# Optimization experiments

Measured on AMD Instinct MI355X. Metric: run time of the kernel, lower is better.

Reference implementation:

```python
import jax, jax.numpy as jnp
import numpy as np

PAD, UNK, START, END = 0, 1, 2, 3


def _lstm_scan(x_tbd, Wih, Whh, b, reverse=False):
    # x_tbd: [T,B,Din]; returns all hidden states [T,B,H] and final hidden [B,H]
    B = x_tbd.shape[1]
    Hh = Whh.shape[1]
    def step(carry, xt):
        h, c = carry
        g = xt @ Wih.T + h @ Whh.T + b  # torch gate order i,f,g,o
        i, f, gg, o = jnp.split(g, 4, axis=-1)
        c = jax.nn.sigmoid(f) * c + jax.nn.sigmoid(i) * jnp.tanh(gg)
        h = jax.nn.sigmoid(o) * jnp.tanh(c)
        return (h, c), h
    z = jnp.zeros((B, Hh), x_tbd.dtype)
    (hT, _), hs = jax.lax.scan(step, (z, z), x_tbd, reverse=reverse)
    return hs, hT


def _forward(fl, input_ids, target_ids, target_lengths):
    (emb,
     eWih0f, eWhh0f, eb0f, eWih0b, eWhh0b, eb0b,
     eWih1f, eWhh1f, eb1f, eWih1b, eWhh1b, eb1b,
     dWih0, dWhh0, db0, dWih1, dWhh1, db1,
     Wenc, Wdec, Wvoc, sW, sb, ob) = fl
    V = emb.shape[0]
    B, S = input_ids.shape
    T = target_ids.shape[1]
    D = 2 * eWhh0f.shape[1]  # decoder hidden = 2*hidden_dim
    safe = lambda ids: jnp.where(ids >= V, UNK, ids)

    # ---- bidirectional 2-layer encoder ----
    x = emb[safe(input_ids)].transpose(1, 0, 2)  # [S,B,E]
    h0f, hf0T = _lstm_scan(x, eWih0f, eWhh0f, eb0f)
    h0b, hb0T = _lstm_scan(x, eWih0b, eWhh0b, eb0b, reverse=True)
    x1 = jnp.concatenate([h0f, h0b], -1)
    h1f, hf1T = _lstm_scan(x1, eWih1f, eWhh1f, eb1f)
    h1b, hb1T = _lstm_scan(x1, eWih1b, eWhh1b, eb1b, reverse=True)
    enc_hs = jnp.concatenate([h1f, h1b], -1).transpose(1, 0, 2)  # [B,S,D]
    # decoder init hidden: concat fwd/bwd final hidden per layer -> [2,B,D]
    dec_h0 = jnp.stack([jnp.concatenate([hf0T, hb0T], -1),
                        jnp.concatenate([hf1T, hb1T], -1)])

    out_proj = jnp.tanh(emb[END:] @ Wvoc)  # [V-3, 3D]
    pad_mask = input_ids == PAD
    t_range = jnp.arange(T)

    def cell(xx, h, c, Wih, Whh, b):
        g = xx @ Wih.T + h @ Whh.T + b
        i, f, gg, o = jnp.split(g, 4, -1)
        c = jax.nn.sigmoid(f) * c + jax.nn.sigmoid(i) * jnp.tanh(gg)
        return jax.nn.sigmoid(o) * jnp.tanh(c), c

    def step(carry, xs):
        h, c, cum, hist, cur, nll = carry
        t, nt = xs  # t scalar step index, nt [B] teacher tokens
        xx = emb[cur]
        h0, c0 = cell(xx, h[0], c[0], dWih0, dWhh0, db0)
        h1, c1 = cell(h0, h[1], c[1], dWih1, dWhh1, db1)
        # intra-temporal encoder attention
        s = jnp.minimum(jnp.einsum('bd,bsd->bs', h1 @ Wenc, enc_hs), 30.0)
        e = jnp.exp(s)
        temporal = e / jnp.where(t == 0, 1.0, cum + 1e-8)
        attn = jax.nn.softmax(jnp.where(pad_mask, -jnp.inf, temporal), axis=1)
        enc_ctx = jnp.einsum('bs,bsd->bd', attn, enc_hs)
        # intra-decoder attention over previous decoder hidden states
        ds = jnp.where(t_range[None, :] < t,
                       jnp.einsum('bd,ubd->bu', h1 @ Wdec, hist), -1e9)
        dec_ctx = jnp.where(t > 0,
                            jnp.einsum('bu,ubd->bd', jax.nn.softmax(ds, axis=1), hist),
                            0.0)
        concat = jnp.concatenate([h1, enc_ctx, dec_ctx], -1)  # [B,3D]
        vocab_dist = jax.nn.softmax(concat @ out_proj.T + ob, axis=1)  # [B,V-3]
        p_gen = jax.nn.sigmoid(concat @ sW.T + sb)[:, 0]
        # generation prob of teacher token (F.pad left by END zeros)
        idx = jnp.clip(nt - END, 0, V - END - 1)
        gen_p = jnp.where((nt >= END) & (nt < V),
                          jnp.take_along_axis(vocab_dist, idx[:, None], 1)[:, 0], 0.0)
        copy_p = jnp.sum(attn * (input_ids == nt[:, None]), axis=1)
        p = p_gen * gen_p + (1.0 - p_gen) * copy_p
        nll = nll - jnp.where(t < target_lengths, jnp.log(p + 1e-9), 0.0)
        return (jnp.stack([h0, h1]), jnp.stack([c0, c1]), cum + e,
                hist.at[t].set(h1), safe(nt), nll), None

    init = (dec_h0, jnp.zeros_like(dec_h0), jnp.zeros((B, S), emb.dtype),
            jnp.zeros((T, B, D), emb.dtype),
            jnp.full((B,), START), jnp.zeros((B,), emb.dtype))
    (_, _, _, _, _, nll), _ = jax.lax.scan(step, init, (t_range, target_ids.T))
    return nll  # per-example teacher-forcing NLL, shape [B]


def setup_inputs():
    key = jax.random.key(0)
    ks = jax.random.split(key, 40)
    B, S, T = 16, 512, 128
    V, E, H = 32000, 128, 256
    D = 2 * H
    inp = {}
    inp['input_ids'] = jax.random.randint(ks[0], (B, S), 4, V)      # no pad/special ids
    inp['target_ids'] = jax.random.randint(ks[1], (B, T), 4, V)
    inp['input_lengths'] = jnp.full((B,), S, dtype=jnp.int32)       # full-length (packing is identity)
    inp['target_lengths'] = jax.random.randint(ks[2], (B,), T // 2, T + 1)
    inp['max_num_oovs'] = 0
    def xav(k, shape):
        fan = shape[0] + shape[-1]
        return jax.random.normal(k, shape, jnp.float32) * np.sqrt(2.0 / fan)
    def lstm_b(n4):
        b = np.zeros(n4, np.float32)
        b[n4 // 4:n4 // 2] = 1.0  # forget-gate bias init
        return jnp.asarray(b)
    i = 3
    inp['emb'] = jax.random.uniform(ks[i], (V, E), jnp.float32, -0.1, 0.1); i += 1
    for l, din in [(0, E), (1, D)]:
        for d in 'fb':
            inp[f'enc_Wih_l{l}{d}'] = xav(ks[i], (4 * H, din)); i += 1
            inp[f'enc_Whh_l{l}{d}'] = xav(ks[i], (4 * H, H)); i += 1
            inp[f'enc_b_l{l}{d}'] = lstm_b(4 * H)
    for l, din in [(0, E), (1, D)]:
        inp[f'dec_Wih_l{l}'] = xav(ks[i], (4 * D, din)); i += 1
        inp[f'dec_Whh_l{l}'] = xav(ks[i], (4 * D, D)); i += 1
        inp[f'dec_b_l{l}'] = lstm_b(4 * D)
    inp['Wenc_attn'] = xav(ks[i], (D, D)); i += 1
    inp['Wdec_attn'] = xav(ks[i], (D, D)); i += 1
    inp['vocab_proj'] = xav(ks[i], (E, 6 * H)); i += 1
    inp['switch_W'] = xav(ks[i], (1, 6 * H)); i += 1
    inp['switch_b'] = jnp.zeros((1,), jnp.float32)
    inp['out_bias'] = jnp.zeros((V - 3,), jnp.float32)
    return inp


def reference(input_ids, target_ids, input_lengths, target_lengths, max_num_oovs,
              emb,
              enc_Wih_l0f, enc_Whh_l0f, enc_b_l0f, enc_Wih_l0b, enc_Whh_l0b, enc_b_l0b,
              enc_Wih_l1f, enc_Whh_l1f, enc_b_l1f, enc_Wih_l1b, enc_Whh_l1b, enc_b_l1b,
              dec_Wih_l0, dec_Whh_l0, dec_b_l0, dec_Wih_l1, dec_Whh_l1, dec_b_l1,
              Wenc_attn, Wdec_attn, vocab_proj, switch_W, switch_b, out_bias):
    # input_lengths unused (all full length -> pack/pad identity); max_num_oovs only
    # widens the zero-padded tail of the generator distribution (gathered probs unchanged).
    fl = (emb,
          enc_Wih_l0f, enc_Whh_l0f, enc_b_l0f, enc_Wih_l0b, enc_Whh_l0b, enc_b_l0b,
          enc_Wih_l1f, enc_Whh_l1f, enc_b_l1f, enc_Wih_l1b, enc_Whh_l1b, enc_b_l1b,
          dec_Wih_l0, dec_Whh_l0, dec_b_l0, dec_Wih_l1, dec_Whh_l1, dec_b_l1,
          Wenc_attn, Wdec_attn, vocab_proj, switch_W, switch_b, out_bias)
    return _forward(fl, input_ids, target_ids, target_lengths)
```

## Files before the change

kernel.cpp:

```cpp
#include <hip/hip_runtime.h>
#include <hip/hip_bf16.h>
#include <math.h>

#define PAD_ID 0
#define UNK_ID 1
#define START_ID 2
#define END_ID 3

constexpr int B = 16, S = 512, T = 128, V = 32000, E = 128, H = 256, D = 512;
constexpr int C3 = 1536;
constexpr int VO = 31997;
constexpr int JS = 32000;

typedef short short8 __attribute__((ext_vector_type(8)));
typedef float f32x4 __attribute__((ext_vector_type(4)));

__device__ __forceinline__ float sigm(float x) { return 1.0f / (1.0f + __expf(-x)); }
__device__ __forceinline__ short bf16s(float x) {
    __hip_bfloat16 h = __float2bfloat16(x);
    return *reinterpret_cast<short*>(&h);
}

__device__ __forceinline__ uint4 cloadu4(const uint* p) {
    uint4 v;
// ... 165 lines not shown
    int tid = threadIdx.x;
    int lane = tid & 63, w = tid >> 6;
    int cl = lane & 15, hi = lane >> 4;

    short8 afr[2][16];
    {
        int rowbase = (bk * 4 + w) * 32;
#pragma unroll
        for (int mt = 0; mt < 2; mt++)
#pragma unroll
            for (int kt = 0; kt < 16; kt++)
                afr[mt][kt] = *(const short8*)(PM + (size_t)(rowbase + mt * 16 + cl) * 512 + kt * 32 + hi * 8);
    }
    if (tid < 128) {
        int g = (tid >> 3) & 3;
        int u = (bk * 4 + (tid >> 5)) * 8 + (tid & 7);
        bias_s[tid] = bs[g * H + u];
    }
    int nl = tid >> 4, kseg = tid & 15;
    int en = tid & 15, rgrp = tid >> 4;
    for (int tt = 0; tt < 32; tt++) {
        int nt = ns * 32 + tt;
        __syncthreads();
        {
            int n = nt * 16 + nl;
            const float* src = (kseg < 8) ? (h0f + (size_t)n * H + kseg * 32)
                                          : (h0b + (size_t)n * H + (kseg - 8) * 32);
            float4 v0 = *(const float4*)(src), v1 = *(const float4*)(src + 4);
            float4 v2 = *(const float4*)(src + 8), v3 = *(const float4*)(src + 12);
            float4 v4 = *(const float4*)(src + 16), v5 = *(const float4*)(src + 20);
            float4 v6 = *(const float4*)(src + 24), v7 = *(const float4*)(src + 28);
            ushort* dst = X + nl * 520 + kseg * 32;
            st_bf8(dst, v0, v1); st_bf8(dst + 8, v2, v3);
            st_bf8(dst + 16, v4, v5); st_bf8(dst + 24, v6, v7);
        }
        __syncthreads();
        {
            f32x4 acc0 = {0.f, 0.f, 0.f, 0.f}, acc1 = {0.f, 0.f, 0.f, 0.f};
            const ushort* hp = X + cl * 520 + hi * 8;
#pragma unroll
            for (int kt = 0; kt < 16; kt++) {
                short8 bfr = *(const short8*)(hp + kt * 32);
                acc0 = __builtin_amdgcn_mfma_f32_16x16x32_bf16(afr[0][kt], bfr, acc0, 0, 0, 0);
                acc1 = __builtin_amdgcn_mfma_f32_16x16x32_bf16(afr[1][kt], bfr, acc1, 0, 0, 0);
            }
#pragma unroll
            for (int i = 0; i < 4; i++) {
                gs[w][hi * 4 + i][cl] = acc0[i];
                gs[w][16 + hi * 4 + i][cl] = acc1[i];
            }
        }
        __syncthreads();
        {
            int wv = rgrp >> 2, g = rgrp & 3;
            int u0 = (bk * 4 + wv) * 8;
            float* dst = G + (size_t)(nt * 16 + en) * 1024 + g * 256 + u0;
            float4 o0, o1;
            o0.x = gs[wv][g * 8 + 0][en] + bias_s[rgrp * 8 + 0];
            o0.y = gs[wv][g * 8 + 1][en] + bias_s[rgrp * 8 + 1];
            o0.z = gs[wv][g * 8 + 2][en] + bias_s[rgrp * 8 + 2];
            o0.w = gs[wv][g * 8 + 3][en] + bias_s[rgrp * 8 + 3];
            o1.x = gs[wv][g * 8 + 4][en] + bias_s[rgrp * 8 + 4];
            o1.y = gs[wv][g * 8 + 5][en] + bias_s[rgrp * 8 + 5];
            o1.z = gs[wv][g * 8 + 6][en] + bias_s[rgrp * 8 + 6];
            o1.w = gs[wv][g * 8 + 7][en] + bias_s[rgrp * 8 + 7];
            *(float4*)dst = o0;
            *(float4*)(dst + 4) = o1;
        }
    }
}


__device__ __forceinline__ void enc_scan_body(int blk, char* smem,
        const float* __restrict__ Gf, const float* __restrict__ Gb,
        const ushort* __restrict__ PMf, const ushort* __restrict__ PMb,
        float* __restrict__ hof, float* __restrict__ hob,
        float* __restrict__ hfin, uint* __restrict__ pk) {
    ushort* hh = (ushort*)smem;
    float (*gs)[32][17] = (float(*)[32][17])(smem + 8448);
    int dirb = blk >> 3, bk = blk & 7;
    const float* G = dirb ? Gb : Gf;
    const ushort* PM = dirb ? PMb : PMf;
    float* ho = dirb ? hob : hof;
    int tid = threadIdx.x;
    int lane = tid & 63, w = tid >> 6;
    int cl = lane & 15, hi = lane >> 4;

    short8 afr[2][8];
    {
        int rowbase = (bk * 4 + w) * 32;
#pragma unroll
        for (int mt = 0; mt < 2; mt++)
#pragma unroll
            for (int kt = 0; kt < 8; kt++)
                afr[mt][kt] = *(const short8*)(PM + (size_t)(rowbase + mt * 16 + cl) * 256 + kt * 32 + hi * 8);
    }
    int ub = tid & 31, bb = tid >> 5;
    int u_glob = bk * 32 + ub;
    int gsw = ub >> 3, ul = ub & 7;
    float c_a = 0.f, c_b = 0.f;
    int b0s = tid >> 4, u0s = (tid & 15) * 16;

    for (int step = 0; step < S; step++) {
        int s = dirb ? (S - 1 - step) : step;
        int cur = step & 1;
        const float* gA = G + ((size_t)(s * B + bb)) * 1024 + u_glob;
        const float* gB = G + ((size_t)(s * B + bb + 8)) * 1024 + u_glob;
        float pa0 = gA[0], pa1 = gA[256], pa2 = gA[512], pa3 = gA[768];
        float pb0 = gB[0], pb1 = gB[256], pb2 = gB[512], pb3 = gB[768];
        poll_stage16(pk + cur * 8192 + dirb * 4096 + tid * 16,
                     (uint)step & 0xffffu, hh + b0s * 264 + u0s);
        __syncthreads();
        {
            f32x4 acc0 = {0.f, 0.f, 0.f, 0.f}, acc1 = {0.f, 0.f, 0.f, 0.f};
            const ushort* hp = hh + cl * 264 + hi * 8;
#pragma unroll
            for (int kt = 0; kt < 8; kt++) {
                short8 bfr = *(const short8*)(hp + kt * 32);
                acc0 = __builtin_amdgcn_mfma_f32_16x16x32_bf16(afr[0][kt], bfr, acc0, 0, 0, 0);
                acc1 = __builtin_amdgcn_mfma_f32_16x16x32_bf16(afr[1][kt], bfr, acc1, 0, 0, 0);
            }
#pragma unroll
            for (int i = 0; i < 4; i++) {
                gs[w][hi * 4 + i][cl] = acc0[i];
                gs[w][16 + hi * 4 + i][cl] = acc1[i];
            }
        }
        __syncthreads();
        {
            float q0 = gs[gsw][0 + ul][bb];
            float q1 = gs[gsw][8 + ul][bb];
            float q2 = gs[gsw][16 + ul][bb];
            float q3 = gs[gsw][24 + ul][bb];
            float ig = sigm(pa0 + q0), fg = sigm(pa1 + q1), gt = tanhf(pa2 + q2), og = sigm(pa3 + q3);
            c_a = fg * c_a + ig * gt;
            float hA = og * tanhf(c_a);
            q0 = gs[gsw][0 + ul][bb + 8];
            q1 = gs[gsw][8 + ul][bb + 8];
            q2 = gs[gsw][16 + ul][bb + 8];
            q3 = gs[gsw][24 + ul][bb + 8];
            ig = sigm(pb0 + q0); fg = sigm(pb1 + q1); gt = tanhf(pb2 + q2); og = sigm(pb3 + q3);
            c_b = fg * c_b + ig * gt;
            float hB = og * tanhf(c_b);
            uint tg = (uint)(step + 1) & 0xffffu;
            uint* dstp = pk + (cur ^ 1) * 8192 + dirb * 4096;
            pstore(&dstp[bb * 256 + u_glob], ((uint)(ushort)bf16s(hA) << 16) | tg);
            pstore(&dstp[(bb + 8) * 256 + u_glob], ((uint)(ushort)bf16s(hB) << 16) | tg);
            ho[((size_t)(s * B + bb)) * H + u_glob] = hA;
            ho[((size_t)(s * B + bb + 8)) * H + u_glob] = hB;
            if (step == S - 1) {
                hfin[bb * (2 * H) + dirb * H + u_glob] = hA;
                hfin[(bb + 8) * (2 * H) + dirb * H + u_glob] = hB;
            }
        }
    }
}

__device__ __forceinline__ void dec0_body(int bid, char* smem,
        const int* __restrict__ tgt, const float* __restrict__ emb,
        const float4* __restrict__ P, const float* __restrict__ bias,
        float* __restrict__ G) {
    float (*xr)[E] = (float(*)[E])smem;
    int n0 = bid * 8;
    int tid = threadIdx.x;
    for (int i = tid; i < 8 * E; i += 256) {
        int r = i >> 7, e = i & 127;
        int n = n0 + r, t = n / B, b = n - t * B;
        int tok;
        if (t == 0) tok = START_ID;
        else { tok = tgt[b * T + (t - 1)]; if (tok >= V) tok = UNK_ID; }
        xr[r][e] = emb[(size_t)tok * E + e];
    }
    __syncthreads();
#pragma unroll
    for (int half = 0; half < 2; half++) {
        int u = tid + half * 256;
        float acc[8][4];
#pragma unroll
        for (int r = 0; r < 8; r++)
#pragma unroll
            for (int g = 0; g < 4; g++) acc[r][g] = 0.f;
#pragma unroll 4
        for (int k = 0; k < E; k++) {
            float4 w = P[k * D + u];
#pragma unroll
            for (int r = 0; r < 8; r++) {
                float x = xr[r][k];
                acc[r][0] += x * w.x; acc[r][1] += x * w.y;
                acc[r][2] += x * w.z; acc[r][3] += x * w.w;
            }
        }
        float b0 = bias[u], b1 = bias[D + u], b2 = bias[2 * D + u], b3 = bias[3 * D + u];
#pragma unroll
        for (int r = 0; r < 8; r++) {
            float* g = G + (size_t)(n0 + r) * (4 * D);
            g[u] = acc[r][0] + b0; g[D + u] = acc[r][1] + b1;
            g[2 * D + u] = acc[r][2] + b2; g[3 * D + u] = acc[r][3] + b3;
        }
    }
}

__device__ __forceinline__ void dec_body(int bk, char* smem,
        const float* __restrict__ G0, const ushort* __restrict__ PM0,
        const ushort* __restrict__ PM1, const float* __restrict__ b1,
        uint* __restrict__ h0pk, uint* __restrict__ h1pk,
        float* __restrict__ h1out) {
    ushort* hb = (ushort*)smem;
    float (*gs)[16][17] = (float(*)[16][17])(smem + 33024);
    int tid = threadIdx.x;
    int lane = tid & 63, w = tid >> 6;
    int cl = lane & 15, hi = lane >> 4;

    short8 a0[16], a1[32];
    {
        const ushort* base0 = PM0 + (size_t)(bk * 64 + w * 16 + cl) * 512 + hi * 8;
#pragma unroll
        for (int kt = 0; kt < 16; kt++) a0[kt] = *(const short8*)(base0 + kt * 32);
        const ushort* base1 = PM1 + (size_t)(bk * 64 + w * 16 + cl) * 1024 + hi * 8;
#pragma unroll
        for (int kt = 0; kt < 32; kt++) a1[kt] = *(const short8*)(base1 + kt * 32);
    }
    int u_loc = tid & 15, b = tid >> 4;
    int u = bk * 16 + u_loc;
    float bi0 = b1[u], bi1 = b1[512 + u], bi2 = b1[1024 + u], bi3 = b1[1536 + u];
    float c0v = 0.f, c1v = 0.f;
    int sb = tid >> 4, kseg = tid & 15;
    int sflat = sb * 512 + kseg * 32;

    for (int t = 0; t < T; t++) {
        int cur = t & 1;
        poll_stage32(h0pk + ((t + 1) & 1) * 8192 + sflat, (uint)(t + 1) & 0xffffu,
                     hb + sb * 1032 + kseg * 32);
        __syncthreads();
        {
            f32x4 acc = {0.f, 0.f, 0.f, 0.f};
            const ushort* hp = hb + cl * 1032 + hi * 8;
#pragma unroll
            for (int kt = 0; kt < 16; kt++) {
                short8 bfr = *(const short8*)(hp + kt * 32);
                acc = __builtin_amdgcn_mfma_f32_16x16x32_bf16(a0[kt], bfr, acc, 0, 0, 0);
            }
#pragma unroll
            for (int i = 0; i < 4; i++) gs[w][hi * 4 + i][cl] = acc[i];
        }
        __syncthreads();
        {
            const float* gg = G0 + ((size_t)(t * B + b)) * 2048 + u;
            float g0 = gg[0]    + gs[0][u_loc][b];
            float g1 = gg[512]  + gs[1][u_loc][b];
            float g2 = gg[1024] + gs[2][u_loc][b];
            float g3 = gg[1536] + gs[3][u_loc][b];
            float ig = sigm(g0), fg = sigm(g1), gt = tanhf(g2), og = sigm(g3);
            c0v = fg * c0v + ig * gt;
            float h0n = og * tanhf(c0v);
            pstore(&h0pk[cur * 8192 + b * 512 + u],
                   ((uint)(ushort)bf16s(h0n) << 16) | ((uint)(t + 2) & 0xffffu));
        }
        poll_stage32(h0pk + cur * 8192 + sflat, (uint)(t + 2) & 0xffffu,
                     hb + sb * 1032 + kseg * 32);
        poll_stage32(h1pk + ((t + 1) & 1) * 8192 + sflat, (uint)(t + 1) & 0xffffu,
                     hb + sb * 1032 + 512 + kseg * 32);
        __syncthreads();
        {
            f32x4 acc = {0.f, 0.f, 0.f, 0.f};
            const ushort* hp = hb + cl * 1032 + hi * 8;
#pragma unroll
            for (int kt = 0; kt < 32; kt++) {
                short8 bfr = *(const short8*)(hp + kt * 32);
                acc = __builtin_amdgcn_mfma_f32_16x16x32_bf16(a1[kt], bfr, acc, 0, 0, 0);
            }
#pragma unroll
            for (int i = 0; i < 4; i++) gs[w][hi * 4 + i][cl] = acc[i];
        }
        __syncthreads();
        {
            float g0 = bi0 + gs[0][u_loc][b];
            float g1 = bi1 + gs[1][u_loc][b];
            float g2 = bi2 + gs[2][u_loc][b];
            float g3 = bi3 + gs[3][u_loc][b];
            float ig = sigm(g0), fg = sigm(g1), gt = tanhf(g2), og = sigm(g3);
            c1v = fg * c1v + ig * gt;
            float h1n = og * tanhf(c1v);
            pstore(&h1pk[cur * 8192 + b * 512 + u],
                   ((uint)(ushort)bf16s(h1n) << 16) | ((uint)(t + 2) & 0xffffu));
            h1out[((size_t)(t * B + b)) * 512 + u] = h1n;
        }
        __syncthreads();
    }
}

__device__ __forceinline__ void encht2_body(int bid,
        const float* __restrict__ h1f, const float* __restrict__ h1b,
        ushort* __restrict__ enchB) {
    int idx = bid * 256 + threadIdx.x;
    int b = idx >> 15;
    int r = idx & 32767;
    int o = r >> 9, s = r & 511;
    const float* src = (o < 32) ? (h1f + ((size_t)(s * B + b)) * H + o * 8)
                                : (h1b + ((size_t)(s * B + b)) * H + (o - 32) * 8);
    float4 v0 = *(const float4*)src, v1 = *(const float4*)(src + 4);
    st_bf8(enchB + ((size_t)b << 18) + o * 4096 + s * 8, v0, v1);
}

__device__ __forceinline__ void outproj_body(int bid, char* smem,
        const float* __restrict__ emb, const float* __restrict__ Wvoc,
        __hip_bfloat16* __restrict__ outT2) {
    float (*er)[E + 1] = (float(*)[E + 1])smem;
    int j0 = bid * 32;
    int jl = threadIdx.x & 31, oq = threadIdx.x >> 5;
    for (int i = threadIdx.x; i < 32 * E; i += 256) {
        int jj = i >> 7, e = i & 127;
        int j = j0 + jj;
        er[jj][e] = (j < VO) ? emb[(size_t)(3 + j) * E + e] : 0.f;
    }
    __syncthreads();
    int j = j0 + jl;
#pragma unroll 1
    for (int i = 0; i < 24; i++) {
        int o = oq * 24 + i;
        int k0 = o * 8;
        float acc[8];
#pragma unroll
        for (int kk = 0; kk < 8; kk++) acc[kk] = 0.f;
#pragma unroll 4
        for (int e = 0; e < E; e++) {
            float x = er[jl][e];
            float4 w0 = *(const float4*)(Wvoc + (size_t)e * C3 + k0);
            float4 w1 = *(const float4*)(Wvoc + (size_t)e * C3 + k0 + 4);
            acc[0] += x * w0.x; acc[1] += x * w0.y; acc[2] += x * w0.z; acc[3] += x * w0.w;
            acc[4] += x * w1.x; acc[5] += x * w1.y; acc[6] += x * w1.z; acc[7] += x * w1.w;
        }
        short8 v;
#pragma unroll
        for (int kk = 0; kk < 8; kk++) v[kk] = bf16s(tanhf(acc[kk]));
        *reinterpret_cast<short8*>((char*)outT2 + ((size_t)o * JS + j) * 16) = v;
    }
}


__global__ void __launch_bounds__(256) megaA(
        const float* Gf, const float* Gb, const ushort* PMf, const ushort* PMb,
        float* hof, float* hob, float* hfin, uint* pk,
        const int* tgt, const float* emb, const float4* PdW, const float* dbias,
        float* Gd0) {
    __shared__ __align__(16) char smem[17152];
    int blk = blockIdx.x;
    if (blk < 16) enc_scan_body(blk, smem, Gf, Gb, PMf, PMb, hof, hob, hfin, pk);
    else dec0_body(blk - 16, smem, tgt, emb, PdW, dbias, Gd0);
}

__global__ void __launch_bounds__(256) enc_pscan3(
        const float* Gf, const float* Gb, const ushort* PMf, const ushort* PMb,
        float* hof, float* hob, float* hfin, uint* pk) {
    __shared__ __align__(16) char smem[17152];
    enc_scan_body(blockIdx.x, smem, Gf, Gb, PMf, PMb, hof, hob, hfin, pk);
}

__global__ void __launch_bounds__(256) megaC(
        const float* G0, const ushort* PM0, const ushort* PM1, const float* b1,
        uint* h0pk, uint* h1pk, float* h1out,
        const float* h1f, const float* h1b, ushort* enchB,
        const float* emb, const float* Wvoc, __hip_bfloat16* outT2) {
    __shared__ __align__(16) char smem[37376];
    int blk = blockIdx.x;
    if (blk < 32) dec_body(blk, smem, G0, PM0, PM1, b1, h0pk, h1pk, h1out);
    else if (blk < 32 + 2048) encht2_body(blk - 32, h1f, h1b, enchB);
    else outproj_body(blk - 2080, smem, emb, Wvoc, outT2);
}

__global__ void dec_initpk(const float* __restrict__ hinit,
                           uint* __restrict__ h0pk, uint* __restrict__ h1pk) {
    int i = blockIdx.x * blockDim.x + threadIdx.x;
    if (i >= B * D) return;
    pstore(&h0pk[8192 + i], ((uint)(ushort)bf16s(hinit[i]) << 16) | 1u);
    pstore(&h1pk[8192 + i], ((uint)(ushort)bf16s(hinit[B * D + i]) << 16) | 1u);
}

__global__ void qproj(const float* __restrict__ h1d, const float* __restrict__ Wenc,
                      const float* __restrict__ Wdec, ushort* __restrict__ qeb16,
                      float* __restrict__ qd) {
    int n = blockIdx.x;
    int o = threadIdx.x;
    __shared__ float hr[D];
    hr[o] = h1d[(size_t)n * D + o];
    __syncthreads();
    float ae = 0.f, ad = 0.f;
#pragma unroll 4
    for (int k = 0; k < D; k++) {
        float hk = hr[k];
        ae += hk * Wenc[k * D + o];
        ad += hk * Wdec[k * D + o];
    }
    int b = n & 15, t = n >> 4;
    qeb16[((size_t)(b * 128 + t) << 9) + o] = (ushort)bf16s(ae);
    qd[(size_t)n * D + o] = ad;
}

__global__ void __launch_bounds__(512) escore_mfma(
        const ushort* __restrict__ qeb16, const ushort* __restrict__ enchB,
        float* __restrict__ ew) {
    __shared__ __align__(16) ushort Bs[2][8192];
    int b = blockIdx.x;
    int tid = threadIdx.x;
    int lane = tid & 63, w = tid >> 6;
    int cl = lane & 15, hi = lane >> 4;
    short8 a[16];
    {
        const ushort* asrc = qeb16 + ((size_t)(b * 128 + w * 16 + cl) << 9) + hi * 8;
#pragma unroll
        for (int kt = 0; kt < 16; kt++) a[kt] = *(const short8*)(asrc + kt * 32);
    }
    const ushort* ebase = enchB + ((size_t)b << 18);
#pragma unroll
    for (int ii = 0; ii < 2; ii++) {
        int c = tid * 2 + ii;
        int o = c >> 4, sl = c & 15;
        gload_lds16(ebase + o * 4096 + sl * 8, (char*)&Bs[0][0] + (size_t)c * 16);
    }
    asm volatile("s_waitcnt vmcnt(0)" ::: "memory");
    __syncthreads();
    int buf = 0;
    for (int st = 0; st < 32; st++) {
        if (st + 1 < 32) {
#pragma unroll
            for (int ii = 0; ii < 2; ii++) {
                int c = tid * 2 + ii;
                int o = c >> 4, sl = c & 15;
                gload_lds16(ebase + o * 4096 + ((st + 1) * 16 + sl) * 8,
                            (char*)&Bs[buf ^ 1][0] + (size_t)c * 16);
            }
        }
        f32x4 acc = {0.f, 0.f, 0.f, 0.f};
        const ushort* bp = &Bs[buf][0] + (hi * 16 + cl) * 8;
#pragma unroll
        for (int kt = 0; kt < 16; kt++) {
            short8 bb = *(const short8*)(bp + kt * 512);
            acc = __builtin_amdgcn_mfma_f32_16x16x32_bf16(a[kt], bb, acc, 0, 0, 0);
        }
        int s = st * 16 + cl;
#pragma unroll
        for (int i = 0; i < 4; i++) {
            int t = w * 16 + hi * 4 + i;
            ew[((size_t)(b * T + t)) * S + s] = __expf(fminf(acc[i], 30.0f));
        }
        asm volatile("s_waitcnt vmcnt(0)" ::: "memory");
        __syncthreads();
        buf ^= 1;
    }
}

__global__ void temporal_k(float* __restrict__ ew) {
    int i = blockIdx.x * blockDim.x + threadIdx.x;
    if (i >= B * S) return;
    int b = i / S, sx = i - b * S;
    float cum = 0.f;
    for (int t = 0; t < T; t++) {
        size_t idx = ((size_t)(b * T + t)) * S + sx;
        float v = ew[idx];
        ew[idx] = v / (t == 0 ? 1.0f : (cum + 1e-8f));
        cum += v;
    }
}

__global__ void attnctx(const float* __restrict__ ew, const int* __restrict__ ids,
                        const int* __restrict__ tgt,
                        const float* __restrict__ h1f, const float* __restrict__ h1b,
                        float* __restrict__ ectx, float* __restrict__ copyp) {
    int bt = blockIdx.x;
    int b = bt / T, t = bt - b * T;
    int tid = threadIdx.x;
    __shared__ float aw[S];
    __shared__ float red[512];
    float v = ew[(size_t)bt * S + tid];
    int tok = ids[b * S + tid];
    bool pad = (tok == PAD_ID);
    float vm = pad ? -INFINITY : v;
    red[tid] = vm; __syncthreads();
    for (int w = 256; w > 0; w >>= 1) { if (tid < w) red[tid] = fmaxf(red[tid], red[tid + w]); __syncthreads(); }
    float m = red[0]; __syncthreads();
    float ex = pad ? 0.f : __expf(vm - m);
    red[tid] = ex; __syncthreads();
    for (int w = 256; w > 0; w >>= 1) { if (tid < w) red[tid] += red[tid + w]; __syncthreads(); }
    float Z = red[0]; __syncthreads();
    float a = ex / Z;
    aw[tid] = a;
    int nt = tgt[b * T + t];
    red[tid] = (tok == nt) ? a : 0.f; __syncthreads();
    for (int w = 256; w > 0; w >>= 1) { if (tid < w) red[tid] += red[tid + w]; __syncthreads(); }
    if (tid == 0) copyp[bt] = red[0];
    __syncthreads();
    int d = tid;
    const float* hp = (d < H) ? (h1f + (size_t)b * H + d) : (h1b + (size_t)b * H + (d - H));
    float acc = 0.f;
#pragma unroll 4
    for (int s2 = 0; s2 < S; s2++) { acc += aw[s2] * hp[0]; hp += B * H; }
    ectx[(size_t)bt * D + d] = acc;
}

__global__ void decattn(const float* __restrict__ qd, const float* __restrict__ h1d,
                        float* __restrict__ dctx) {
    int bt = blockIdx.x;
    int b = bt / T, t = bt - b * T;
    int tid = threadIdx.x;
    __shared__ float q[D];
    __shared__ float wl[T];
    __shared__ float red[128];
    for (int i = tid; i < D; i += 128) q[i] = qd[((size_t)(t * B + b)) * D + i];
    __syncthreads();
    float sc = -INFINITY;
    if (tid < t) {
        const float* hu = h1d + ((size_t)(tid * B + b)) * D;
        float a = 0.f;
#pragma unroll 4
        for (int k = 0; k < D; k++) a += q[k] * hu[k];
        sc = a;
    }
    red[tid] = sc; __syncthreads();
    for (int w = 64; w > 0; w >>= 1) { if (tid < w) red[tid] = fmaxf(red[tid], red[tid + w]); __syncthreads(); }
    float m = red[0]; __syncthreads();
    float ex = (tid < t) ? __expf(sc - m) : 0.f;
    red[tid] = ex; __syncthreads();
    for (int w = 64; w > 0; w >>= 1) { if (tid < w) red[tid] += red[tid + w]; __syncthreads(); }
    float Z = red[0]; __syncthreads();
    wl[tid] = (t > 0) ? (ex / Z) : 0.f;
    __syncthreads();
    for (int d = tid; d < D; d += 128) {
        float acc = 0.f;
        for (int u = 0; u < t; u++) acc += wl[u] * h1d[((size_t)(u * B + b)) * D + d];
        dctx[(size_t)bt * D + d] = acc;
    }
}

__global__ void concat_k(const float* __restrict__ h1d, const float* __restrict__ ectx,
                         const float* __restrict__ dctx, const float* __restrict__ sW,
                         const float* __restrict__ sb, ushort* __restrict__ ccb16,
                         float* __restrict__ pgen) {
    int bt = blockIdx.x;
    int b = bt / T, t = bt - b * T;
    int d = threadIdx.x;
    __shared__ float red[512];
    float v0 = h1d[((size_t)(t * B + b)) * D + d];
    float v1 = ectx[(size_t)bt * D + d];
    float v2 = dctx[(size_t)bt * D + d];
    ushort* c = ccb16 + (size_t)bt * C3;
    c[d] = (ushort)bf16s(v0); c[D + d] = (ushort)bf16s(v1); c[2 * D + d] = (ushort)bf16s(v2);
    red[d] = v0 * sW[d] + v1 * sW[D + d] + v2 * sW[2 * D + d];
    __syncthreads();
    for (int w = 256; w > 0; w >>= 1) { if (d < w) red[d] += red[d + w]; __syncthreads(); }
    if (d == 0) pgen[bt] = 1.f / (1.f + __expf(-(red[0] + sb[0])));
}

__global__ void __launch_bounds__(512) vocab_mfma3(
        const __hip_bfloat16* __restrict__ outT2, const ushort* __restrict__ ccb16,
        const float* __restrict__ ob, const int* __restrict__ tgt,
        float* __restrict__ pbuf) {
    __shared__ __align__(16) ushort Bs[2][3072 * 8];
    __shared__ int jstar_s[128];
    int bid = blockIdx.x;
    int rb = bid & 15, jg = bid >> 4;
    int row0 = rb * 128;
    int tid = threadIdx.x;
    int lane = tid & 63, w = tid >> 6;
    int cl = lane & 15, hi = lane >> 4;
    int j0base = jg * 2000;

    if (tid < 128) {
        int nt = tgt[row0 + tid];
        int ix = nt - 3;
        ix = ix < 0 ? 0 : (ix > VO - 1 ? VO - 1 : ix);
        jstar_s[tid] = ix;
    }
    short8 a[48];
    {
        const ushort* asrc = ccb16 + (size_t)(row0 + w * 16 + cl) * C3 + hi * 8;
#pragma unroll
        for (int kt = 0; kt < 48; kt++) a[kt] = *(const short8*)(asrc + kt * 32);
    }
    {
#pragma unroll
        for (int ii = 0; ii < 6; ii++) {
            int c = w * 384 + ii * 64 + lane;
            int o = c >> 4, jl = c & 15;
            const char* g = (const char*)outT2 + ((size_t)o * JS + (size_t)(j0base + jl)) * 16;
            gload_lds16(g, (char*)&Bs[0][0] + (size_t)(w * 384 + ii * 64) * 16);
        }
    }
    asm volatile("s_waitcnt vmcnt(0)" ::: "memory");
    __syncthreads();
    int jst[4];
    float m[4], sacc[4], gl[4];
#pragma unroll
    for (int i = 0; i < 4; i++) {
        jst[i] = jstar_s[w * 16 + hi * 4 + i];
        m[i] = -1e30f; sacc[i] = 0.f; gl[i] = -1e30f;
    }
    int buf = 0;
    for (int t = 0; t < 125; t++) {
        if (t + 1 < 125) {
            int j0 = j0base + (t + 1) * 16;
#pragma unroll
            for (int ii = 0; ii < 6; ii++) {
                int c = w * 384 + ii * 64 + lane;
                int o = c >> 4, jl = c & 15;
                const char* g = (const char*)outT2 + ((size_t)o * JS + (size_t)(j0 + jl)) * 16;
                gload_lds16(g, (char*)&Bs[buf ^ 1][0] + (size_t)(w * 384 + ii * 64) * 16);
            }
        }
        f32x4 acc = {0.f, 0.f, 0.f, 0.f};
        const ushort* bp = &Bs[buf][0] + (size_t)(hi * 16 + cl) * 8;
#pragma unroll
        for (int kt = 0; kt < 48; kt++) {
            short8 b = *(const short8*)(bp + (size_t)kt * 512);
            acc = __builtin_amdgcn_mfma_f32_16x16x32_bf16(a[kt], b, acc, 0, 0, 0);
        }
        int j = j0base + t * 16 + cl;
        bool valid = j < VO;
        float obj = valid ? ob[j] : 0.f;
#pragma unroll
        for (int i = 0; i < 4; i++) {
            float L = acc[i] + obj;
            if (valid) {
                if (j == jst[i]) gl[i] = L;
                float mn = fmaxf(m[i], L);
                sacc[i] = sacc[i] * __expf(m[i] - mn) + __expf(L - mn);
                m[i] = mn;
            }
        }
        asm volatile("s_waitcnt vmcnt(0)" ::: "memory");
        __syncthreads();
        buf ^= 1;
    }
#pragma unroll
    for (int i = 0; i < 4; i++) {
        for (int mask = 1; mask < 16; mask <<= 1) {
            float om = __shfl_xor(m[i], mask);
            float os = __shfl_xor(sacc[i], mask);
            float mn = fmaxf(m[i], om);
            sacc[i] = sacc[i] * __expf(m[i] - mn) + os * __expf(om - mn);
            m[i] = mn;
            gl[i] = fmaxf(gl[i], __shfl_xor(gl[i], mask));
        }
    }
    if (cl == 0) {
#pragma unroll
        for (int i = 0; i < 4; i++) {
            int rl = w * 16 + hi * 4 + i;
            float* o = pbuf + ((size_t)(jg * 16 + rb) * 128 + rl) * 4;
            o[0] = m[i]; o[1] = sacc[i]; o[2] = gl[i];
        }
    }
}

__global__ void combine_nll_k(const float* __restrict__ pbuf, const int* __restrict__ tgt,
                              const float* __restrict__ pgen, const float* __restrict__ copyp,
                              const int* __restrict__ tlen, float* __restrict__ out) {
    int b = blockIdx.x, t = threadIdx.x;
    int row = b * T + t;
    int rb = row >> 7, rl = row & 127;
    float M = -1e30f, SS = 0.f, GL = -1e30f;
#pragma unroll
    for (int q = 0; q < 16; q++) {
        const float* p = pbuf + ((size_t)(q * 16 + rb) * 128 + rl) * 4;
        float mq = p[0], sq = p[1], gq = p[2];
        float mn = fmaxf(M, mq);
        SS = SS * __expf(M - mn) + sq * __expf(mq - mn);
        M = mn;
        GL = fmaxf(GL, gq);
    }
    int nt = tgt[row];
    float genp = (nt >= 3 && nt < V) ? __expf(GL - M) / SS : 0.f;
    float pg = pgen[row];
    float p = pg * genp + (1.f - pg) * copyp[row];
    __shared__ float red[128];
    red[t] = (t < tlen[b]) ? -logf(p + 1e-9f) : 0.f;
    __syncthreads();
    for (int w = 64; w > 0; w >>= 1) { if (t < w) red[t] += red[t + w]; __syncthreads(); }
    if (t == 0) out[b] = red[0];
}

extern "C" void kernel_launch(void* const* d_in, const int* in_sizes, int n_in,
                              void* d_out, int out_size, void* d_ws, size_t ws_size,
                              hipStream_t stream) {
    const int* input_ids = (const int*)d_in[0];
    const int* target_ids = (const int*)d_in[1];
    const int* tlen = (const int*)d_in[3];
    const float* emb = (const float*)d_in[5];
    const float* eWih0f = (const float*)d_in[6],  *eWhh0f = (const float*)d_in[7],  *eb0f = (const float*)d_in[8];
    const float* eWih0b = (const float*)d_in[9],  *eWhh0b = (const float*)d_in[10], *eb0b = (const float*)d_in[11];
    const float* eWih1f = (const float*)d_in[12], *eWhh1f = (const float*)d_in[13], *eb1f = (const float*)d_in[14];
    const float* eWih1b = (const float*)d_in[15], *eWhh1b = (const float*)d_in[16], *eb1b = (const float*)d_in[17];
    const float* dWih0 = (const float*)d_in[18], *dWhh0 = (const float*)d_in[19], *db0 = (const float*)d_in[20];
    const float* dWih1 = (const float*)d_in[21], *dWhh1 = (const float*)d_in[22], *db1 = (const float*)d_in[23];
    const float* Wenc = (const float*)d_in[24], *Wdec = (const float*)d_in[25];
    const float* Wvoc = (const float*)d_in[26], *sW = (const float*)d_in[27], *sb = (const float*)d_in[28];
    const float* ob = (const float*)d_in[29];
    float* out = (float*)d_out;
    (void)ws_size; (void)n_in; (void)in_sizes; (void)out_size;

    char* A = (char*)d_ws;
    float4* pWih0f = (float4*)(A + 0);
    float4* pWih0b = (float4*)(A + 524288);
    ushort* PMW1f  = (ushort*)(A + 1048576);
    ushort* PMW1b  = (ushort*)(A + 2097152);
    float4* pdWih0 = (float4*)(A + 5242880);
    ushort* PMf0  = (ushort*)(A + 6291456);
    ushort* PMb0  = (ushort*)(A + 6815744);
    ushort* PMf1  = (ushort*)(A + 7340032);
    ushort* PMb1  = (ushort*)(A + 7864320);
    float* G0f = (float*)(A + 23068672);
    float* G0b = (float*)(A + 56623104);
    __hip_bfloat16* outT2 = (__hip_bfloat16*)A;

    char* Bh = A + 98304000;
    float* h0f = (float*)(Bh + 0);
    float* h0b = (float*)(Bh + 8388608);
    float* h1d = (float*)(Bh + 0);
    ushort* qeb16 = (ushort*)(Bh + 4194304);
    float* qd  = (float*)(Bh + 8388608);
    float* ew  = (float*)(Bh + 12582912);
    float* pbuf = (float*)(Bh + 12582912);

    char* Cr = Bh + 16777216;
    float* h1f = (float*)(Cr + 0);
    float* h1b = (float*)(Cr + 8388608);
    ushort* ccb16 = (ushort*)(Cr + 16777216);
    float* dec_init = (float*)(Cr + 29360128);
    float* pgen  = (float*)(Cr + 29425664);
    float* copyp = (float*)(Cr + 29433856);
    uint* hpkE0  = (uint*)(Cr + 29769728);
    uint* hpkE1  = (uint*)(Cr + 29835264);
    uint* h0pkD  = (uint*)(Cr + 29900800);
    uint* h1pkD  = (uint*)(Cr + 29966336);

    char* X = Cr + 30031872;
    float*  Gd0x  = (float*)(X + 0);
    ushort* PM0x  = (ushort*)(X + 16777216);
    ushort* PM1x  = (ushort*)(X + 18874368);
    ushort* enchB = (ushort*)(X + 23068672);
    float*  ectx  = (float*)(X + 31457280);
    float*  dctx  = (float*)(X + 35651584);

    hipMemsetAsync(hpkE0, 0, 262144, stream);

    auto pack = [&](const float* W, float4* P, int Hn, int K) {
        int total = Hn * K;
        hipLaunchKernelGGL(pack4_kernel, dim3((total + 255) / 256), dim3(256), 0, stream, W, P, Hn, K);
    };
    pack(eWih0f, pWih0f, H, E);
    pack(eWih0b, pWih0b, H, E);
    pack(dWih0, pdWih0, D, E);
    hipLaunchKernelGGL(packencMK_k, dim3(4 * H * 256 / 256), dim3(256), 0, stream, eWhh0f, PMf0, 256);
    hipLaunchKernelGGL(packencMK_k, dim3(4 * H * 256 / 256), dim3(256), 0, stream, eWhh0b, PMb0, 256);
    hipLaunchKernelGGL(packencMK_k, dim3(4 * H * 256 / 256), dim3(256), 0, stream, eWhh1f, PMf1, 256);
    hipLaunchKernelGGL(packencMK_k, dim3(4 * H * 256 / 256), dim3(256), 0, stream, eWhh1b, PMb1, 256);
    hipLaunchKernelGGL(packencMK_k, dim3(4 * H * 512 / 256), dim3(256), 0, stream, eWih1f, PMW1f, 512);
    hipLaunchKernelGGL(packencMK_k, dim3(4 * H * 512 / 256), dim3(256), 0, stream, eWih1b, PMW1b, 512);
    hipLaunchKernelGGL(packdecM_k, dim3(4 * D * D / 256), dim3(256), 0, stream, dWhh0, PM0x);
    hipLaunchKernelGGL(packdecM2_k, dim3(8 * D * D / 256), dim3(256), 0, stream, dWih1, dWhh1, PM1x);

    hipLaunchKernelGGL(enc0_gates2, dim3(S * B / 8), dim3(256), 0, stream,
                       input_ids, emb, pWih0f, eb0f, pWih0b, eb0b, G0f, G0b);
    hipLaunchKernelGGL(megaA, dim3(272), dim3(256), 0, stream,
                       G0f, G0b, PMf0, PMb0, h0f, h0b, dec_init, hpkE0,
                       target_ids, emb, pdWih0, db0, Gd0x);
    hipLaunchKernelGGL(enc1g_mfma, dim3(256), dim3(256), 0, stream,
                       h0f, h0b, PMW1f, PMW1b, eb1f, eb1b, G0f, G0b);
    hipLaunchKernelGGL(enc_pscan3, dim3(16), dim3(256), 0, stream,
                       G0f, G0b, PMf1, PMb1, h1f, h1b, dec_init + B * D, hpkE1);
    hipLaunchKernelGGL(dec_initpk, dim3(B * D / 256), dim3(256), 0, stream,
                       dec_init, h0pkD, h1pkD);
    hipLaunchKernelGGL(megaC, dim3(3080), dim3(256), 0, stream,
                       Gd0x, PM0x, PM1x, db1, h0pkD, h1pkD, h1d,
                       h1f, h1b, enchB, emb, Wvoc, outT2);
    hipLaunchKernelGGL(qproj, dim3(T * B), dim3(D), 0, stream, h1d, Wenc, Wdec, qeb16, qd);
    hipLaunchKernelGGL(escore_mfma, dim3(16), dim3(512), 0, stream, qeb16, enchB, ew);
    hipLaunchKernelGGL(temporal_k, dim3((B * S + 255) / 256), dim3(256), 0, stream, ew);
    hipLaunchKernelGGL(attnctx, dim3(B * T), dim3(S), 0, stream,
                       ew, input_ids, target_ids, h1f, h1b, ectx, copyp);
    hipLaunchKernelGGL(decattn, dim3(B * T), dim3(T), 0, stream, qd, h1d, dctx);
    hipLaunchKernelGGL(concat_k, dim3(B * T), dim3(D), 0, stream,
                       h1d, ectx, dctx, sW, sb, ccb16, pgen);
    hipLaunchKernelGGL(vocab_mfma3, dim3(256), dim3(512), 0, stream,
                       outT2, ccb16, ob, target_ids, pbuf);
    hipLaunchKernelGGL(combine_nll_k, dim3(B), dim3(T), 0, stream,
                       pbuf, target_ids, pgen, copyp, tlen, out);
}
```

Before: 4.157 ms.

## Move attention scores, softmax and context products to bf16 MFMA GEMMs

Replaces the scalar per-(b,t) attention context loops (attnctx, decattn) with a shared MFMA GEMM template. Encoder context and decoder self-attention scores and context now run as batched bf16 GEMMs over packed transposed operands (enchT, h1dB1, h1dB2). Softmax is split into a separate kernel that writes bf16 weights. The aim is to remove the serial S-length and t-length FMA loops that re-read fp32 hidden states per block. In exchange it adds packing passes, extra buffers and bf16 rounding of the attention weights and queries.

```diff
diff --git a/kernel.cpp b/kernel.cpp
--- a/kernel.cpp
+++ b/kernel.cpp
@@ -491,6 +491,24 @@
     st_bf8(enchB + ((size_t)b << 18) + o * 4096 + s * 8, v0, v1);
 }
 
+__device__ __forceinline__ void encht2T_body(int bid,
+        const float* __restrict__ h1f, const float* __restrict__ h1b,
+        ushort* __restrict__ enchT) {
+    int idx = bid * 256 + threadIdx.x;
+    int b = idx >> 15;
+    int r = idx & 32767;
+    int o = r >> 9, d = r & 511;
+    float f[8];
+#pragma unroll
+    for (int j = 0; j < 8; j++) {
+        int s = o * 8 + j;
+        f[j] = (d < H) ? h1f[((size_t)(s * B + b)) * H + d]
+                       : h1b[((size_t)(s * B + b)) * H + (d - H)];
+    }
+    float4 v0 = {f[0], f[1], f[2], f[3]}, v1 = {f[4], f[5], f[6], f[7]};
+    st_bf8(enchT + ((size_t)b << 18) + o * 4096 + d * 8, v0, v1);
+}
+
 __device__ __forceinline__ void outproj_body(int bid, char* smem,
         const float* __restrict__ emb, const float* __restrict__ Wvoc,
         __hip_bfloat16* __restrict__ outT2) {
@@ -526,6 +544,61 @@
     }
 }
 
+template<int NF, int TILES, int OSTR, bool DOEXP>
+__device__ __forceinline__ void gemm16_body(char* smem,
+        const ushort* __restrict__ Abase, int arow_stride,
+        const ushort* __restrict__ Bsrc, float* __restrict__ outbase,
+        int out_stride) {
+    ushort* Bs = (ushort*)smem;
+    const int CH = NF * 64;
+    const int NG = CH / 64;
+    int tid = threadIdx.x;
+    int lane = tid & 63, w = tid >> 6;
+    int cl = lane & 15, hi = lane >> 4;
+    short8 a[NF];
+    {
+        const ushort* asrc = Abase + (size_t)(w * 16 + cl) * arow_stride + hi * 8;
+#pragma unroll
+        for (int kt = 0; kt < NF; kt++) a[kt] = *(const short8*)(asrc + kt * 32);
+    }
+    for (int g = w; g < NG; g += 8) {
+        int c = g * 64 + lane;
+        int o = c >> 4, jl = c & 15;
+        gload_lds16(Bsrc + ((size_t)o * OSTR + jl) * 8,
+                    (char*)Bs + (size_t)(g * 64) * 16);
+    }
+    asm volatile("s_waitcnt vmcnt(0)" ::: "memory");
+    __syncthreads();
+    int buf = 0;
+    for (int t = 0; t < TILES; t++) {
+        if (t + 1 < TILES) {
+            for (int g = w; g < NG; g += 8) {
+                int c = g * 64 + lane;
+                int o = c >> 4, jl = c & 15;
+                gload_lds16(Bsrc + ((size_t)o * OSTR + (t + 1) * 16 + jl) * 8,
+                            (char*)Bs + (size_t)((buf ^ 1) * CH + g * 64) * 16);
+            }
+        }
+        f32x4 acc = {0.f, 0.f, 0.f, 0.f};
+        const ushort* bp = Bs + (size_t)buf * CH * 8 + (size_t)(hi * 16 + cl) * 8;
+#pragma unroll
+        for (int kt = 0; kt < NF; kt++) {
+            short8 b = *(const short8*)(bp + (size_t)kt * 512);
+            acc = __builtin_amdgcn_mfma_f32_16x16x32_bf16(a[kt], b, acc, 0, 0, 0);
+        }
+#pragma unroll
+        for (int i = 0; i < 4; i++) {
+            int row = w * 16 + hi * 4 + i;
+            float v = acc[i];
+            if (DOEXP) v = __expf(fminf(v, 30.0f));
+            outbase[(size_t)row * out_stride + t * 16 + cl] = v;
+        }
+        asm volatile("s_waitcnt vmcnt(0)" ::: "memory");
+        __syncthreads();
+        buf ^= 1;
+    }
+}
+
 
 __global__ void __launch_bounds__(256) megaA(
         const float* Gf, const float* Gb, const ushort* PMf, const ushort* PMb,
@@ -548,13 +621,14 @@
 __global__ void __launch_bounds__(256) megaC(
         const float* G0, const ushort* PM0, const ushort* PM1, const float* b1,
         uint* h0pk, uint* h1pk, float* h1out,
-        const float* h1f, const float* h1b, ushort* enchB,
+        const float* h1f, const float* h1b, ushort* enchB, ushort* enchT,
         const float* emb, const float* Wvoc, __hip_bfloat16* outT2) {
     __shared__ __align__(16) char smem[37376];
     int blk = blockIdx.x;
     if (blk < 32) dec_body(blk, smem, G0, PM0, PM1, b1, h0pk, h1pk, h1out);
-    else if (blk < 32 + 2048) encht2_body(blk - 32, h1f, h1b, enchB);
-    else outproj_body(blk - 2080, smem, emb, Wvoc, outT2);
+    else if (blk < 2080) encht2_body(blk - 32, h1f, h1b, enchB);
+    else if (blk < 4128) encht2T_body(blk - 2080, h1f, h1b, enchT);
+    else outproj_body(blk - 4128, smem, emb, Wvoc, outT2);
 }
 
 __global__ void dec_initpk(const float* __restrict__ hinit,
@@ -567,7 +641,7 @@
 
 __global__ void qproj(const float* __restrict__ h1d, const float* __restrict__ Wenc,
                       const float* __restrict__ Wdec, ushort* __restrict__ qeb16,
-                      float* __restrict__ qd) {
+                      ushort* __restrict__ qdb16, ushort* __restrict__ h1dB1) {
     int n = blockIdx.x;
     int o = threadIdx.x;
     __shared__ float hr[D];
@@ -581,60 +655,48 @@
         ad += hk * Wdec[k * D + o];
     }
     int b = n & 15, t = n >> 4;
-    qeb16[((size_t)(b * 128 + t) << 9) + o] = (ushort)bf16s(ae);
-    qd[(size_t)n * D + o] = ad;
-}
-
-__global__ void __launch_bounds__(512) escore_mfma(
+    size_t rowb = (size_t)(b * 128 + t) << 9;
+    qeb16[rowb + o] = (ushort)bf16s(ae);
+    qdb16[rowb + o] = (ushort)bf16s(ad);
+    if (o < 64) {
+        float4 v0 = *(const float4*)(hr + o * 8);
+        float4 v1 = *(const float4*)(hr + o * 8 + 4);
+        st_bf8(h1dB1 + ((size_t)b << 16) + o * 1024 + t * 8, v0, v1);
+    }
+}
+
+__global__ void pack_h1dB2(const float* __restrict__ h1d, ushort* __restrict__ h1dB2) {
+    int idx = blockIdx.x * 256 + threadIdx.x;
+    int b = idx >> 13;
+    int r = idx & 8191;
+    int o = r >> 9, d = r & 511;
+    float f[8];
+#pragma unroll
+    for (int j = 0; j < 8; j++)
+        f[j] = h1d[((size_t)((o * 8 + j) * B + b)) * D + d];
+    float4 v0 = {f[0], f[1], f[2], f[3]}, v1 = {f[4], f[5], f[6], f[7]};
+    st_bf8(h1dB2 + ((size_t)b << 16) + o * 4096 + d * 8, v0, v1);
+}
+
+__global__ void __launch_bounds__(512) scoreAB(
         const ushort* __restrict__ qeb16, const ushort* __restrict__ enchB,
-        float* __restrict__ ew) {
-    __shared__ __align__(16) ushort Bs[2][8192];
-    int b = blockIdx.x;
-    int tid = threadIdx.x;
-    int lane = tid & 63, w = tid >> 6;
-    int cl = lane & 15, hi = lane >> 4;
-    short8 a[16];
-    {
-        const ushort* asrc = qeb16 + ((size_t)(b * 128 + w * 16 + cl) << 9) + hi * 8;
-#pragma unroll
-        for (int kt = 0; kt < 16; kt++) a[kt] = *(const short8*)(asrc + kt * 32);
-    }
-    const ushort* ebase = enchB + ((size_t)b << 18);
-#pragma unroll
-    for (int ii = 0; ii < 2; ii++) {
-        int c = tid * 2 + ii;
-        int o = c >> 4, sl = c & 15;
-        gload_lds16(ebase + o * 4096 + sl * 8, (char*)&Bs[0][0] + (size_t)c * 16);
-    }
-    asm volatile("s_waitcnt vmcnt(0)" ::: "memory");
-    __syncthreads();
-    int buf = 0;
-    for (int st = 0; st < 32; st++) {
-        if (st + 1 < 32) {
-#pragma unroll
-            for (int ii = 0; ii < 2; ii++) {
-                int c = tid * 2 + ii;
-                int o = c >> 4, sl = c & 15;
-                gload_lds16(ebase + o * 4096 + ((st + 1) * 16 + sl) * 8,
-                            (char*)&Bs[buf ^ 1][0] + (size_t)c * 16);
-            }
-        }
-        f32x4 acc = {0.f, 0.f, 0.f, 0.f};
-        const ushort* bp = &Bs[buf][0] + (hi * 16 + cl) * 8;
-#pragma unroll
-        for (int kt = 0; kt < 16; kt++) {
-            short8 bb = *(const short8*)(bp + kt * 512);
-            acc = __builtin_amdgcn_mfma_f32_16x16x32_bf16(a[kt], bb, acc, 0, 0, 0);
-        }
-        int s = st * 16 + cl;
-#pragma unroll
-        for (int i = 0; i < 4; i++) {
-            int t = w * 16 + hi * 4 + i;
-            ew[((size_t)(b * T + t)) * S + s] = __expf(fminf(acc[i], 30.0f));
-        }
-        asm volatile("s_waitcnt vmcnt(0)" ::: "memory");
-        __syncthreads();
-        buf ^= 1;
+        float* __restrict__ ew,
+        const ushort* __restrict__ qdb16, const ushort* __restrict__ h1dB1,
+        float* __restrict__ dsout) {
+    __shared__ __align__(16) char smem[32768];
+    int blk = blockIdx.x;
+    if (blk < 16) {
+        int b = blk;
+        gemm16_body<16, 32, 512, true>(smem,
+            qeb16 + ((size_t)(b * 128) << 9), 512,
+            enchB + ((size_t)b << 18),
+            ew + (size_t)b * T * S, S);
+    } else {
+        int b = blk - 16;
+        gemm16_body<16, 8, 128, false>(smem,
+            qdb16 + ((size_t)(b * 128) << 9), 512,
+            h1dB1 + ((size_t)b << 16),
+            dsout + ((size_t)(b * 128)) * 128, 128);
     }
 }
 
@@ -651,72 +713,71 @@
     }
 }
 
-__global__ void attnctx(const float* __restrict__ ew, const int* __restrict__ ids,
-                        const int* __restrict__ tgt,
-                        const float* __restrict__ h1f, const float* __restrict__ h1b,
-                        float* __restrict__ ectx, float* __restrict__ copyp) {
-    int bt = blockIdx.x;
-    int b = bt / T, t = bt - b * T;
+__global__ void __launch_bounds__(512) smAB(
+        const float* __restrict__ ew, const int* __restrict__ ids,
+        const int* __restrict__ tgt, ushort* __restrict__ awb16,
+        float* __restrict__ copyp,
+        const float* __restrict__ dsout, ushort* __restrict__ pdb16) {
+    __shared__ float red[512];
+    int blk = blockIdx.x;
     int tid = threadIdx.x;
-    __shared__ float aw[S];
-    __shared__ float red[512];
-    float v = ew[(size_t)bt * S + tid];
-    int tok = ids[b * S + tid];
-    bool pad = (tok == PAD_ID);
-    float vm = pad ? -INFINITY : v;
-    red[tid] = vm; __syncthreads();
-    for (int w = 256; w > 0; w >>= 1) { if (tid < w) red[tid] = fmaxf(red[tid], red[tid + w]); __syncthreads(); }
-    float m = red[0]; __syncthreads();
-    float ex = pad ? 0.f : __expf(vm - m);
-    red[tid] = ex; __syncthreads();
-    for (int w = 256; w > 0; w >>= 1) { if (tid < w) red[tid] += red[tid + w]; __syncthreads(); }
-    float Z = red[0]; __syncthreads();
-    float a = ex / Z;
-    aw[tid] = a;
-    int nt = tgt[b * T + t];
-    red[tid] = (tok == nt) ? a : 0.f; __syncthreads();
-    for (int w = 256; w > 0; w >>= 1) { if (tid < w) red[tid] += red[tid + w]; __syncthreads(); }
-    if (tid == 0) copyp[bt] = red[0];
-    __syncthreads();
-    int d = tid;
-    const float* hp = (d < H) ? (h1f + (size_t)b * H + d) : (h1b + (size_t)b * H + (d - H));
-    float acc = 0.f;
-#pragma unroll 4
-    for (int s2 = 0; s2 < S; s2++) { acc += aw[s2] * hp[0]; hp += B * H; }
-    ectx[(size_t)bt * D + d] = acc;
-}
-
-__global__ void decattn(const float* __restrict__ qd, const float* __restrict__ h1d,
-                        float* __restrict__ dctx) {
-    int bt = blockIdx.x;
-    int b = bt / T, t = bt - b * T;
-    int tid = threadIdx.x;
-    __shared__ float q[D];
-    __shared__ float wl[T];
-    __shared__ float red[128];
-    for (int i = tid; i < D; i += 128) q[i] = qd[((size_t)(t * B + b)) * D + i];
-    __syncthreads();
-    float sc = -INFINITY;
-    if (tid < t) {
-        const float* hu = h1d + ((size_t)(tid * B + b)) * D;
-        float a = 0.f;
-#pragma unroll 4
-        for (int k = 0; k < D; k++) a += q[k] * hu[k];
-        sc = a;
-    }
-    red[tid] = sc; __syncthreads();
-    for (int w = 64; w > 0; w >>= 1) { if (tid < w) red[tid] = fmaxf(red[tid], red[tid + w]); __syncthreads(); }
-    float m = red[0]; __syncthreads();
-    float ex = (tid < t) ? __expf(sc - m) : 0.f;
-    red[tid] = ex; __syncthreads();
-    for (int w = 64; w > 0; w >>= 1) { if (tid < w) red[tid] += red[tid + w]; __syncthreads(); }
-    float Z = red[0]; __syncthreads();
-    wl[tid] = (t > 0) ? (ex / Z) : 0.f;
-    __syncthreads();
-    for (int d = tid; d < D; d += 128) {
-        float acc = 0.f;
-        for (int u = 0; u < t; u++) acc += wl[u] * h1d[((size_t)(u * B + b)) * D + d];
-        dctx[(size_t)bt * D + d] = acc;
+    if (blk < 2048) {
+        int bt = blk;
+        int b = bt >> 7, t = bt & 127;
+        float v = ew[(size_t)bt * S + tid];
+        int tok = ids[b * S + tid];
+        bool pad = (tok == PAD_ID);
+        float vm = pad ? -INFINITY : v;
+        red[tid] = vm; __syncthreads();
+        for (int w = 256; w > 0; w >>= 1) { if (tid < w) red[tid] = fmaxf(red[tid], red[tid + w]); __syncthreads(); }
+        float m = red[0]; __syncthreads();
+        float ex = pad ? 0.f : __expf(vm - m);
+        red[tid] = ex; __syncthreads();
+        for (int w = 256; w > 0; w >>= 1) { if (tid < w) red[tid] += red[tid + w]; __syncthreads(); }
+        float Z = red[0]; __syncthreads();
+        float a = ex / Z;
+        int nt = tgt[b * T + t];
+        red[tid] = (tok == nt) ? a : 0.f; __syncthreads();
+        for (int w = 256; w > 0; w >>= 1) { if (tid < w) red[tid] += red[tid + w]; __syncthreads(); }
+        if (tid == 0) copyp[bt] = red[0];
+        awb16[(size_t)bt * S + tid] = (ushort)bf16s(a);
+    } else {
+        int bt2 = blk - 2048;
+        int t = bt2 & 127;
+        float sc = -INFINITY;
+        if (tid < 128 && tid < t) sc = dsout[(size_t)bt2 * 128 + tid];
+        if (tid < 128) red[tid] = sc;
+        __syncthreads();
+        for (int w = 64; w > 0; w >>= 1) { if (tid < w) red[tid] = fmaxf(red[tid], red[tid + w]); __syncthreads(); }
+        float m = red[0]; __syncthreads();
+        float ex = (tid < 128 && tid < t) ? __expf(sc - m) : 0.f;
+        if (tid < 128) red[tid] = ex;
+        __syncthreads();
+        for (int w = 64; w > 0; w >>= 1) { if (tid < w) red[tid] += red[tid + w]; __syncthreads(); }
+        float Z = red[0];
+        if (tid < 128) pdb16[(size_t)bt2 * 128 + tid] = (ushort)bf16s((t > 0) ? ex / Z : 0.f);
+    }
+}
+
+__global__ void __launch_bounds__(512) ctxAB(
+        const ushort* __restrict__ awb16, const ushort* __restrict__ enchT,
+        float* __restrict__ ectx,
+        const ushort* __restrict__ pdb16, const ushort* __restrict__ h1dB2,
+        float* __restrict__ dctx) {
+    __shared__ __align__(16) char smem[32768];
+    int blk = blockIdx.x;
+    if (blk < 16) {
+        int b = blk;
+        gemm16_body<16, 32, 512, false>(smem,
+            awb16 + ((size_t)(b * 128)) * 512, 512,
+            enchT + ((size_t)b << 18),
+            ectx + ((size_t)(b * 128)) * 512, 512);
+    } else {
+        int b = blk - 16;
+        gemm16_body<4, 32, 512, false>(smem,
+            pdb16 + ((size_t)(b * 128)) * 128, 128,
+            h1dB2 + ((size_t)b << 16),
+            dctx + ((size_t)(b * 128)) * 512, 512);
     }
 }
 
@@ -905,7 +966,9 @@
     float* h0b = (float*)(Bh + 8388608);
     float* h1d = (float*)(Bh + 0);
     ushort* qeb16 = (ushort*)(Bh + 4194304);
-    float* qd  = (float*)(Bh + 8388608);
+    ushort* awb16 = (ushort*)(Bh + 6291456);
+    ushort* qdb16 = (ushort*)(Bh + 8388608);
+    ushort* h1dB1 = (ushort*)(Bh + 10485760);
     float* ew  = (float*)(Bh + 12582912);
     float* pbuf = (float*)(Bh + 12582912);
 
@@ -913,6 +976,9 @@
     float* h1f = (float*)(Cr + 0);
     float* h1b = (float*)(Cr + 8388608);
     ushort* ccb16 = (ushort*)(Cr + 16777216);
+    float*  dsout = (float*)(Cr + 23068672);
+    ushort* pdb16 = (ushort*)(Cr + 24117248);
+    ushort* h1dB2 = (ushort*)(Cr + 24641536);
     float* dec_init = (float*)(Cr + 29360128);
     float* pgen  = (float*)(Cr + 29425664);
     float* copyp = (float*)(Cr + 29433856);
@@ -928,6 +994,7 @@
     ushort* enchB = (ushort*)(X + 23068672);
     float*  ectx  = (float*)(X + 31457280);
     float*  dctx  = (float*)(X + 35651584);
+    ushort* enchT = (ushort*)(X + 39845888);
 
     hipMemsetAsync(hpkE0, 0, 262144, stream);
 
@@ -958,15 +1025,19 @@
                        G0f, G0b, PMf1, PMb1, h1f, h1b, dec_init + B * D, hpkE1);
     hipLaunchKernelGGL(dec_initpk, dim3(B * D / 256), dim3(256), 0, stream,
                        dec_init, h0pkD, h1pkD);
-    hipLaunchKernelGGL(megaC, dim3(3080), dim3(256), 0, stream,
+    hipLaunchKernelGGL(megaC, dim3(5128), dim3(256), 0, stream,
                        Gd0x, PM0x, PM1x, db1, h0pkD, h1pkD, h1d,
-                       h1f, h1b, enchB, emb, Wvoc, outT2);
-    hipLaunchKernelGGL(qproj, dim3(T * B), dim3(D), 0, stream, h1d, Wenc, Wdec, qeb16, qd);
-    hipLaunchKernelGGL(escore_mfma, dim3(16), dim3(512), 0, stream, qeb16, enchB, ew);
+                       h1f, h1b, enchB, enchT, emb, Wvoc, outT2);
+    hipLaunchKernelGGL(qproj, dim3(T * B), dim3(D), 0, stream,
+                       h1d, Wenc, Wdec, qeb16, qdb16, h1dB1);
+    hipLaunchKernelGGL(pack_h1dB2, dim3(512), dim3(256), 0, stream, h1d, h1dB2);
+    hipLaunchKernelGGL(scoreAB, dim3(32), dim3(512), 0, stream,
+                       qeb16, enchB, ew, qdb16, h1dB1, dsout);
     hipLaunchKernelGGL(temporal_k, dim3((B * S + 255) / 256), dim3(256), 0, stream, ew);
-    hipLaunchKernelGGL(attnctx, dim3(B * T), dim3(S), 0, stream,
-                       ew, input_ids, target_ids, h1f, h1b, ectx, copyp);
-    hipLaunchKernelGGL(decattn, dim3(B * T), dim3(T), 0, stream, qd, h1d, dctx);
+    hipLaunchKernelGGL(smAB, dim3(4096), dim3(512), 0, stream,
+                       ew, input_ids, target_ids, awb16, copyp, dsout, pdb16);
+    hipLaunchKernelGGL(ctxAB, dim3(32), dim3(512), 0, stream,
+                       awb16, enchT, ectx, pdb16, h1dB2, dctx);
     hipLaunchKernelGGL(concat_k, dim3(B * T), dim3(D), 0, stream,
                        h1d, ectx, dctx, sW, sb, ccb16, pgen);
     hipLaunchKernelGGL(vocab_mfma3, dim3(256), dim3(512), 0, stream,
```

Result: faster. 4.003 ms (-3.7%).
